# Performance work log

Hardware: AMD Instinct MI355X
Metric: run time of the kernel (lower is better)

The kernel has to match this reference:

```python
import jax, jax.numpy as jnp
import numpy as np

B, S, T, D, H, K, F = 8, 512, 512, 1024, 16, 64, 4096
EPS = 1e-6
NEG = -1e9


def _ln(x, g, b):
    mu = jnp.mean(x, axis=-1, keepdims=True)
    var = jnp.mean(jnp.square(x - mu), axis=-1, keepdims=True)
    return (x - mu) * jax.lax.rsqrt(var + EPS) * g + b


def _mha(q_in, kv_in, wq, bq, wk, bk, wv, bv, wo, bo, mask=None):
    # q_in: [B,S,D], kv_in: [B,T,D]
    q = jnp.einsum('bsd,dhk->bshk', q_in, wq) + bq
    k = jnp.einsum('btd,dhk->bthk', kv_in, wk) + bk
    v = jnp.einsum('btd,dhk->bthk', kv_in, wv) + bv
    scores = jnp.einsum('bshk,bthk->bhst', q, k) / jnp.sqrt(jnp.float32(K))
    if mask is not None:
        scores = jnp.where(mask, scores, NEG)
    attn = jax.nn.softmax(scores, axis=-1)  # [B,H,S,T]
    ctx = jnp.einsum('bhst,bthk->bshk', attn, v)
    out = jnp.einsum('bshk,hkd->bsd', ctx, wo) + bo
    return out, attn


def setup_inputs() -> dict:
    key = jax.random.key(0)
    ks = jax.random.split(key, 24)
    r = lambda i, shape: 0.02 * jax.random.normal(ks[i], shape, dtype=jnp.float32)
    inp = {
        'x': jax.random.normal(ks[0], (B, S, D), dtype=jnp.float32),
        'enc_output': jax.random.normal(ks[1], (B, T, D), dtype=jnp.float32),
        'look_ahead_mask': jnp.tril(jnp.ones((S, S), dtype=bool))[None, None],
        # mha1 (self-attention)
        'wq1': r(2, (D, H, K)), 'bq1': jnp.zeros((H, K), jnp.float32),
        'wk1': r(3, (D, H, K)), 'bk1': jnp.zeros((H, K), jnp.float32),
        'wv1': r(4, (D, H, K)), 'bv1': jnp.zeros((H, K), jnp.float32),
        'wo1': r(5, (H, K, D)), 'bo1': jnp.zeros((D,), jnp.float32),
        # mha2 (cross-attention)
        'wq2': r(6, (D, H, K)), 'bq2': jnp.zeros((H, K), jnp.float32),
        'wk2': r(7, (D, H, K)), 'bk2': jnp.zeros((H, K), jnp.float32),
        'wv2': r(8, (D, H, K)), 'bv2': jnp.zeros((H, K), jnp.float32),
        'wo2': r(9, (H, K, D)), 'bo2': jnp.zeros((D,), jnp.float32),
        # layernorms
        'g1': jnp.ones((D,), jnp.float32), 'be1': jnp.zeros((D,), jnp.float32),
        'g2': jnp.ones((D,), jnp.float32), 'be2': jnp.zeros((D,), jnp.float32),
        'g3': jnp.ones((D,), jnp.float32), 'be3': jnp.zeros((D,), jnp.float32),
        # ffn
        'w_fc1': r(10, (D, F)), 'b_fc1': jnp.zeros((F,), jnp.float32),
        'w_fc2': r(11, (F, D)), 'b_fc2': jnp.zeros((D,), jnp.float32),
    }
    return inp


def reference(x, enc_output, look_ahead_mask,
              wq1, bq1, wk1, bk1, wv1, bv1, wo1, bo1,
              wq2, bq2, wk2, bk2, wv2, bv2, wo2, bo2,
              g1, be1, g2, be2, g3, be3,
              w_fc1, b_fc1, w_fc2, b_fc2):
    attn1, attn_w1 = _mha(x, x, wq1, bq1, wk1, bk1, wv1, bv1, wo1, bo1,
                          mask=look_ahead_mask)
    out1 = _ln(attn1 + x, g1, be1)
    attn2, attn_w2 = _mha(out1, enc_output, wq2, bq2, wk2, bk2, wv2, bv2, wo2, bo2)
    out2 = _ln(attn2 + out1, g2, be2)
    h = jax.nn.relu(jnp.einsum('bsd,df->bsf', out2, w_fc1) + b_fc1)
    out_ffn = jnp.einsum('bsf,fd->bsd', h, w_fc2) + b_fc2
    dec_layer_out = _ln(out_ffn + out2, g3, be3)
    return dec_layer_out, attn_w1, attn_w2
```

## Files before the change

### kernel.cpp

```cpp
#include <hip/hip_runtime.h>

typedef __attribute__((ext_vector_type(4))) float f32x4;
typedef __attribute__((ext_vector_type(8))) __bf16 bf16x8;

__device__ __forceinline__ unsigned short f2b(float f){
  union { float f; unsigned int u; } v; v.f = f;
  unsigned int r = v.u + 0x7FFFu + ((v.u >> 16) & 1u);
  return (unsigned short)(r >> 16);
}
__device__ __forceinline__ float b2f(unsigned short u){
  union { unsigned int u; float f; } v; v.u = ((unsigned int)u) << 16;
  return v.f;
}
__device__ __forceinline__ bool in_is_bf16(const void* g1){
  return ((const unsigned short*)g1)[0] == 0x3F80u;
}

#define GLD16(gp, lp) __builtin_amdgcn_global_load_lds( \
    (const __attribute__((address_space(1))) unsigned int*)(gp), \
    (__attribute__((address_space(3))) unsigned int*)(lp), 16, 0, 0)

__device__ __forceinline__ int xcd_swz(int L, int nwg){
  return (L & 7) * (nwg >> 3) + (L >> 3);
}

__global__ __launch_bounds__(256) void k_fill(float* p, long long n, float v){
  long long i = (long long)blockIdx.x*256 + threadIdx.x;
  long long stride = (long long)gridDim.x*256;
  for(; i < n; i += stride) p[i] = v;
}

struct SmallConv { const void* src[16]; int n[16]; int off[16]; };
struct TW4 { const void* s[4]; };

template<bool SMALL>
__global__ __launch_bounds__(256) void k_prepA(SmallConv sc, float* bias,
    const void* act_in, unsigned short* act_out,
    TW4 tw, unsigned short* wdst, const void* g1f)
{
  __shared__ float tile[32][33];
  bool isb = in_is_bf16(g1f);
  int bi = blockIdx.x, tid = threadIdx.x;
  int base = SMALL ? 16 : 0;
  if(SMALL && bi < 16){
    const void* s = sc.src[bi];
    float* d = bias + sc.off[bi];
    int n = sc.n[bi];
    for(int j=tid;j<n;j+=256)
      d[j] = isb ? b2f(((const unsigned short*)s)[j]) : ((const float*)s)[j];
  } else if(bi < base + 2048){
    for(int i=(bi-base)*256+tid; i<4194304; i+=2048*256){
      float v = isb ? b2f(((const unsigned short*)act_in)[i]) : ((const float*)act_in)[i];
      act_out[i] = f2b(v);
    }
  } else {
    int r = bi - (base + 2048);
    int wi = r >> 10, rem = r & 1023;
    int c0 = (rem & 31)*32, r0 = (rem >> 5)*32;
    const void* src = tw.s[wi];
    unsigned short* dst = wdst + (size_t)wi*1048576;
    int tx = tid & 31, ty = tid >> 5;
    for(int rr=ty; rr<32; rr+=8){
      size_t o = (size_t)(r0+rr)*1024 + c0 + tx;
      tile[rr][tx] = isb ? b2f(((const unsigned short*)src)[o]) : ((const float*)src)[o];
    }
    __syncthreads();
    for(int cc=ty; cc<32; cc+=8)
      dst[(size_t)(c0+cc)*1024 + r0 + tx] = f2b(tile[tx][cc]);
  }
}

__global__ __launch_bounds__(256) void k_prep3(
    const void* fc1, unsigned short* fc1t,
    const void* fc2, unsigned short* fc2t, const void* g1f)
{
  __shared__ float tile[32][33];
  bool isb = in_is_bf16(g1f);
  int bi = blockIdx.x, tid = threadIdx.x;
  const void* src; unsigned short* dst; int R, C, bx, by;
  if(bi < 4096){ src = fc1; dst = fc1t; R = 1024; C = 4096; bx = bi & 127; by = bi >> 7; }
  else { int r = bi - 4096; src = fc2; dst = fc2t; R = 4096; C = 1024; bx = r & 31; by = r >> 5; }
  int c0 = bx*32, r0 = by*32;
  int tx = tid & 31, ty = tid >> 5;
  for(int rr=ty; rr<32; rr+=8){
    size_t o = (size_t)(r0+rr)*C + c0 + tx;
    tile[rr][tx] = isb ? b2f(((const unsigned short*)src)[o]) : ((const float*)src)[o];
  }
  __syncthreads();
  for(int cc=ty; cc<32; cc+=8)
    dst[(size_t)(c0+cc)*R + r0 + tx] = f2b(tile[tx][cc]);
}

template<int EPI>
__global__ __launch_bounds__(256) void k_gemm(
    const unsigned short* __restrict__ A, int lda,
    const unsigned short* __restrict__ Bt, int ldb,
    void* __restrict__ Cout, int ldc,
    const float* __restrict__ bias, const unsigned short* __restrict__ resid, int K)
{
  __shared__ unsigned short As[2][128*32];
  __shared__ unsigned short Bs[2][128*32];
  int tid = threadIdx.x;
  int lane = tid & 63, w = tid >> 6;
  int lr = lane & 15, lg = lane >> 4;
  int nwg = gridDim.x * gridDim.y;
  int v = xcd_swz(blockIdx.y * gridDim.x + blockIdx.x, nwg);
  int bx = v % gridDim.x, by = v / gridDim.x;
  int m0 = by * 128, n0 = bx * 128;
  int wr = w >> 1, wc = w & 1;

  f32x4 acc[4][4];
  #pragma unroll
  for(int m=0;m<4;m++)
    #pragma unroll
    for(int n=0;n<4;n++) acc[m][n] = (f32x4){0.f,0.f,0.f,0.f};

  #pragma unroll
  for(int j=0;j<2;j++){
    int idx = j*256 + tid;
    GLD16(A + (size_t)(m0 + (idx>>2))*lda + (idx&3)*8,
          As[0] + (size_t)(j*256 + (tid & 192))*8);
    GLD16(Bt + (size_t)(n0 + (idx>>2))*ldb + (idx&3)*8,
          Bs[0] + (size_t)(j*256 + (tid & 192))*8);
  }
  __syncthreads();

  int cur = 0;
  for(int k0 = 0; k0 < K; k0 += 32){
    if(k0 + 32 < K){
      #pragma unroll
      for(int j=0;j<2;j++){
        int idx = j*256 + tid;
        GLD16(A + (size_t)(m0 + (idx>>2))*lda + k0 + 32 + (idx&3)*8,
              As[cur^1] + (size_t)(j*256 + (tid & 192))*8);
        GLD16(Bt + (size_t)(n0 + (idx>>2))*ldb + k0 + 32 + (idx&3)*8,
              Bs[cur^1] + (size_t)(j*256 + (tid & 192))*8);
      }
    }
    bf16x8 a[4], b[4];
    #pragma unroll
    for(int m=0;m<4;m++) a[m] = *(const bf16x8*)&As[cur][(wr*64 + m*16 + lr)*32 + lg*8];
    #pragma unroll
    for(int n=0;n<4;n++) b[n] = *(const bf16x8*)&Bs[cur][(wc*64 + n*16 + lr)*32 + lg*8];
    #pragma unroll
    for(int m=0;m<4;m++)
      #pragma unroll
      for(int n=0;n<4;n++)
        acc[m][n] = __builtin_amdgcn_mfma_f32_16x16x32_bf16(a[m], b[n], acc[m][n], 0,0,0);
    __syncthreads();
    cur ^= 1;
  }

  #pragma unroll
  for(int m=0;m<4;m++){
    #pragma unroll
    for(int n=0;n<4;n++){
      int col = n0 + wc*64 + n*16 + lr;
      float bb = bias[col];
      #pragma unroll
      for(int r=0;r<4;r++){
        int row = m0 + wr*64 + m*16 + lg*4 + r;
        size_t o = (size_t)row*ldc + col;
        float v2 = acc[m][n][r] + bb;
        if constexpr (EPI == 0){
          ((unsigned short*)Cout)[o] = f2b(v2);
        } else if constexpr (EPI == 1){
          ((unsigned short*)Cout)[o] = f2b(v2 > 0.f ? v2 : 0.f);
        } else if constexpr (EPI == 2){
          ((unsigned short*)Cout)[o] = f2b(v2 + b2f(resid[o]));
        } else {
          ((float*)Cout)[o] = v2 + b2f(resid[o]);
        }
      }
    }
  }
}

template<int EPI>
__global__ __launch_bounds__(256) void k_gemm64(
    const unsigned short* __restrict__ A, int lda,
    const unsigned short* __restrict__ Bt, int ldb,
    void* __restrict__ Cout, int ldc,
    const float* __restrict__ bias, const unsigned short* __restrict__ resid, int K)
{
  __shared__ unsigned short As[2][128*32];
  __shared__ unsigned short Bs[2][64*32];
  int tid = threadIdx.x, lane = tid & 63, w = tid >> 6;
  int lr = lane & 15, lg = lane >> 4;
  int nwg = gridDim.x * gridDim.y;
  int v = xcd_swz(blockIdx.y * gridDim.x + blockIdx.x, nwg);
  int bx = v % gridDim.x, by = v / gridDim.x;
  int m0 = by * 128, n0 = bx * 64;

  f32x4 acc[2][4];
  #pragma unroll
  for(int m=0;m<2;m++)
    #pragma unroll
    for(int n=0;n<4;n++) acc[m][n] = (f32x4){0.f,0.f,0.f,0.f};

  #pragma unroll
  for(int j=0;j<2;j++){
    int idx = j*256 + tid;
    GLD16(A + (size_t)(m0 + (idx>>2))*lda + (idx&3)*8,
          As[0] + (size_t)(j*256 + (tid & 192))*8);
  }
  GLD16(Bt + (size_t)(n0 + (tid>>2))*ldb + (tid&3)*8,
        Bs[0] + (size_t)(tid & 192)*8);
  __syncthreads();

  int cur = 0;
  for(int k0 = 0; k0 < K; k0 += 32){
    if(k0 + 32 < K){
      #pragma unroll
      for(int j=0;j<2;j++){
        int idx = j*256 + tid;
        GLD16(A + (size_t)(m0 + (idx>>2))*lda + k0 + 32 + (idx&3)*8,
              As[cur^1] + (size_t)(j*256 + (tid & 192))*8);
      }
      GLD16(Bt + (size_t)(n0 + (tid>>2))*ldb + k0 + 32 + (tid&3)*8,
            Bs[cur^1] + (size_t)(tid & 192)*8);
    }
    bf16x8 a[2], bf[4];
    #pragma unroll
    for(int m=0;m<2;m++) a[m] = *(const bf16x8*)&As[cur][(w*32 + m*16 + lr)*32 + lg*8];
    #pragma unroll
    for(int n=0;n<4;n++) bf[n] = *(const bf16x8*)&Bs[cur][(n*16 + lr)*32 + lg*8];
    #pragma unroll
    for(int m=0;m<2;m++)
      #pragma unroll
      for(int n=0;n<4;n++)
        acc[m][n] = __builtin_amdgcn_mfma_f32_16x16x32_bf16(a[m], bf[n], acc[m][n], 0,0,0);
    __syncthreads();
    cur ^= 1;
  }

  #pragma unroll
  for(int m=0;m<2;m++){
    #pragma unroll
    for(int n=0;n<4;n++){
      int col = n0 + n*16 + lr;
      float bb = bias[col];
      #pragma unroll
      for(int r=0;r<4;r++){
        int row = m0 + w*32 + m*16 + lg*4 + r;
        size_t o = (size_t)row*ldc + col;
        float v2 = acc[m][n][r] + bb;
        if constexpr (EPI == 0){
          ((unsigned short*)Cout)[o] = f2b(v2);
        } else if constexpr (EPI == 1){
          ((unsigned short*)Cout)[o] = f2b(v2 > 0.f ? v2 : 0.f);
        } else if constexpr (EPI == 2){
          ((unsigned short*)Cout)[o] = f2b(v2 + b2f(resid[o]));
        } else {
          ((float*)Cout)[o] = v2 + b2f(resid[o]);
        }
      }
    }
  }
}

template<int TSLOT>
__global__ __launch_bounds__(256) void k_gemmsplit(
    const unsigned short* __restrict__ A, int lda,
    const unsigned short* __restrict__ Bt, int ldb,
    unsigned short* __restrict__ C0, unsigned short* __restrict__ C1,
    unsigned short* __restrict__ C2,
    const float* __restrict__ bias, int K)
{
  __shared__ unsigned short As[2][128*32];
  __shared__ unsigned short Bs[2][128*32];
  int tid = threadIdx.x;
  int lane = tid & 63, w = tid >> 6;
  int lr = lane & 15, lg = lane >> 4;
  int nwg = gridDim.x * gridDim.y;
  int v = xcd_swz(blockIdx.y * gridDim.x + blockIdx.x, nwg);
  int bx = v % gridDim.x, by = v / gridDim.x;
  int m0 = by * 128, n0 = bx * 128;
  int wr = w >> 1, wc = w & 1;
  int slot = n0 >> 10;
  unsigned short* Cs = slot == 0 ? C0 : (slot == 1 ? C1 : C2);
  int nl0 = n0 & 1023;

  f32x4 acc[4][4];
  #pragma unroll
  for(int m=0;m<4;m++)
    #pragma unroll
    for(int n=0;n<4;n++) acc[m][n] = (f32x4){0.f,0.f,0.f,0.f};

  #pragma unroll
  for(int j=0;j<2;j++){
    int idx = j*256 + tid;
    GLD16(A + (size_t)(m0 + (idx>>2))*lda + (idx&3)*8,
          As[0] + (size_t)(j*256 + (tid & 192))*8);
    GLD16(Bt + (size_t)(n0 + (idx>>2))*ldb + (idx&3)*8,
          Bs[0] + (size_t)(j*256 + (tid & 192))*8);
  }
  __syncthreads();

  int cur = 0;
  for(int k0 = 0; k0 < K; k0 += 32){
    if(k0 + 32 < K){
      #pragma unroll
      for(int j=0;j<2;j++){
        int idx = j*256 + tid;
        GLD16(A + (size_t)(m0 + (idx>>2))*lda + k0 + 32 + (idx&3)*8,
              As[cur^1] + (size_t)(j*256 + (tid & 192))*8);
        GLD16(Bt + (size_t)(n0 + (idx>>2))*ldb + k0 + 32 + (idx&3)*8,
              Bs[cur^1] + (size_t)(j*256 + (tid & 192))*8);
      }
    }
    bf16x8 a[4], b[4];
    #pragma unroll
    for(int m=0;m<4;m++) a[m] = *(const bf16x8*)&As[cur][(wr*64 + m*16 + lr)*32 + lg*8];
    #pragma unroll
    for(int n=0;n<4;n++) b[n] = *(const bf16x8*)&Bs[cur][(wc*64 + n*16 + lr)*32 + lg*8];
    #pragma unroll
    for(int m=0;m<4;m++)
      #pragma unroll
      for(int n=0;n<4;n++)
        acc[m][n] = __builtin_amdgcn_mfma_f32_16x16x32_bf16(a[m], b[n], acc[m][n], 0,0,0);
    __syncthreads();
    cur ^= 1;
  }

  if(slot != TSLOT){
    #pragma unroll
    for(int m=0;m<4;m++){
      #pragma unroll
      for(int n=0;n<4;n++){
        int coll = nl0 + wc*64 + n*16 + lr;
        float bb = bias[n0 + wc*64 + n*16 + lr];
        #pragma unroll
        for(int r=0;r<4;r++){
          int row = m0 + wr*64 + m*16 + lg*4 + r;
          Cs[(size_t)row*1024 + coll] = f2b(acc[m][n][r] + bb);
        }
      }
    }
  } else {
    #pragma unroll
    for(int m=0;m<4;m++){
      #pragma unroll
      for(int n=0;n<4;n++){
        int vcol = nl0 + wc*64 + n*16 + lr;
        float bb = bias[n0 + wc*64 + n*16 + lr];
        int rowb = m0 + wr*64 + m*16 + lg*4;
        int z = (rowb >> 9)*16 + (vcol >> 6);
        unsigned short tmp[4];
        #pragma unroll
        for(int r=0;r<4;r++) tmp[r] = f2b(acc[m][n][r] + bb);
        *(ushort4*)&Cs[((size_t)(z*64 + (vcol & 63)))*512 + (rowb & 511)] = *(ushort4*)tmp;
      }
    }
  }
}

template<bool CAUSAL>
__global__ __launch_bounds__(256) void k_attnf(
    const unsigned short* Q,
    const unsigned short* __restrict__ Km,
    const unsigned short* __restrict__ Vt,
    float* __restrict__ P,
    unsigned short* C)
{
  int tid = threadIdx.x, lane = tid & 63, w = tid >> 6;
  int lr = lane & 15, lg = lane >> 4;
  int L = (blockIdx.z * 16 + blockIdx.y) * 16 + blockIdx.x;
  int v = xcd_swz(L, 2048);
  int s0 = (v & 15) * 32;
  int h = (v >> 4) & 15;
  int b = v >> 8;
  int z = b*16 + h;
  const unsigned short* Qb = Q + ((size_t)(b*512 + s0))*1024 + h*64;
  const unsigned short* Kb = Km + ((size_t)(b*512))*1024 + h*64;
  float* Pb = P + ((size_t)(z*512 + s0))*512;

  __shared__ unsigned short P_lds[32*520];
  __shared__ float redm[32][4];
  __shared__ float reds[32][4];

  bf16x8 aq[2][2];
  #pragma unroll
  for(int m=0;m<2;m++)
    #pragma unroll
    for(int kk=0;kk<2;kk++)
      aq[m][kk] = *(const bf16x8*)(Qb + (size_t)(m*16 + lr)*1024 + kk*32 + lg*8);

  f32x4 sc[2][8];
  #pragma unroll
  for(int m=0;m<2;m++)
    #pragma unroll
    for(int cb=0;cb<8;cb++) sc[m][cb] = (f32x4){0.f,0.f,0.f,0.f};

  #pragma unroll
  for(int cb=0; cb<8; cb++){
    int col = w*128 + cb*16 + lr;
    #pragma unroll
    for(int kk=0; kk<2; kk++){
      bf16x8 bq = *(const bf16x8*)(Kb + (size_t)col*1024 + kk*32 + lg*8);
      #pragma unroll
      for(int m=0;m<2;m++)
        sc[m][cb] = __builtin_amdgcn_mfma_f32_16x16x32_bf16(aq[m][kk], bq, sc[m][cb], 0,0,0);
    }
  }

  #pragma unroll
  for(int m=0;m<2;m++)
    #pragma unroll
    for(int cb=0;cb<8;cb++)
      #pragma unroll
      for(int r=0;r<4;r++){
        int row_l = m*16 + lg*4 + r;
        int col = w*128 + cb*16 + lr;
        float sv = sc[m][cb][r] * 0.125f;
        if(CAUSAL && col > s0 + row_l) sv = -1e9f;
        sc[m][cb][r] = sv;
      }

  float gmax[2][4];
  #pragma unroll
  for(int m=0;m<2;m++)
    #pragma unroll
    for(int r=0;r<4;r++){
      float pm = -1e30f;
      #pragma unroll
      for(int cb=0;cb<8;cb++) pm = fmaxf(pm, sc[m][cb][r]);
      #pragma unroll
      for(int off=1; off<16; off<<=1) pm = fmaxf(pm, __shfl_xor(pm, off));
      if(lr == 0) redm[m*16 + lg*4 + r][w] = pm;
    }
  __syncthreads();
  #pragma unroll
  for(int m=0;m<2;m++)
    #pragma unroll
    for(int r=0;r<4;r++){
      int row_l = m*16 + lg*4 + r;
      gmax[m][r] = fmaxf(fmaxf(redm[row_l][0], redm[row_l][1]),
                         fmaxf(redm[row_l][2], redm[row_l][3]));
    }
  #pragma unroll
  for(int m=0;m<2;m++)
    #pragma unroll
    for(int r=0;r<4;r++){
      float ps = 0.f;
      #pragma unroll
      for(int cb=0;cb<8;cb++){
        float e = __expf(sc[m][cb][r] - gmax[m][r]);
        sc[m][cb][r] = e;
        ps += e;
      }
      #pragma unroll
      for(int off=1; off<16; off<<=1) ps += __shfl_xor(ps, off);
      if(lr == 0) reds[m*16 + lg*4 + r][w] = ps;
    }
  __syncthreads();
  #pragma unroll
  for(int m=0;m<2;m++)
    #pragma unroll
    for(int r=0;r<4;r++){
      int row_l = m*16 + lg*4 + r;
      float inv = 1.f / (reds[row_l][0] + reds[row_l][1] + reds[row_l][2] + reds[row_l][3]);
      #pragma unroll
      for(int cb=0;cb<8;cb++){
        int col = w*128 + cb*16 + lr;
        float p = sc[m][cb][r] * inv;
        Pb[(size_t)row_l*512 + col] = p;
        P_lds[row_l*520 + col] = f2b(p);
      }
    }
  __syncthreads();

  const unsigned short* Vb = Vt + ((size_t)z*64 + w*16 + lr)*512;
  f32x4 pacc[2];
  pacc[0] = (f32x4){0.f,0.f,0.f,0.f};
  pacc[1] = (f32x4){0.f,0.f,0.f,0.f};
  for(int kk = 0; kk < 16; kk++){
    bf16x8 bfrag = *(const bf16x8*)(Vb + kk*32 + lg*8);
    #pragma unroll
    for(int m=0;m<2;m++){
      bf16x8 afrag = *(const bf16x8*)&P_lds[(m*16 + lr)*520 + kk*32 + lg*8];
      pacc[m] = __builtin_amdgcn_mfma_f32_16x16x32_bf16(afrag, bfrag, pacc[m], 0,0,0);
    }
  }
  #pragma unroll
  for(int m=0;m<2;m++)
    #pragma unroll
    for(int r=0;r<4;r++)
      C[((size_t)(b*512 + s0 + m*16 + lg*4 + r))*1024 + h*64 + w*16 + lr] = f2b(pacc[m][r]);
}

template<int F32IN, int F32OUT>
__global__ __launch_bounds__(256) void k_ln(const void* __restrict__ in,
    const float* __restrict__ g, const float* __restrict__ be,
    void* __restrict__ out)
{
  int row = blockIdx.x, tid = threadIdx.x;
  float v[4];
  if constexpr (F32IN){
    f32x4 u = *(const f32x4*)((const float*)in + (size_t)row*1024 + tid*4);
    v[0]=u[0]; v[1]=u[1]; v[2]=u[2]; v[3]=u[3];
  } else {
    uint2 u = *(const uint2*)((const unsigned short*)in + (size_t)row*1024 + tid*4);
    v[0] = b2f(u.x & 0xFFFF); v[1] = b2f(u.x >> 16);
    v[2] = b2f(u.y & 0xFFFF); v[3] = b2f(u.y >> 16);
  }
  float s = v[0]+v[1]+v[2]+v[3];
  float s2 = v[0]*v[0]+v[1]*v[1]+v[2]*v[2]+v[3]*v[3];
  #pragma unroll
  for(int off=1; off<64; off<<=1){ s += __shfl_xor(s, off); s2 += __shfl_xor(s2, off); }
  __shared__ float red[2][4];
  int w = tid >> 6;
  if((tid & 63) == 0){ red[0][w] = s; red[1][w] = s2; }
  __syncthreads();
  s  = red[0][0]+red[0][1]+red[0][2]+red[0][3];
  s2 = red[1][0]+red[1][1]+red[1][2]+red[1][3];
  float mu = s * (1.f/1024.f);
  float var = s2 * (1.f/1024.f) - mu*mu;
  float rstd = rsqrtf(var + 1e-6f);
  int c = tid*4;
  float y0 = (v[0]-mu)*rstd*g[c+0] + be[c+0];
  float y1 = (v[1]-mu)*rstd*g[c+1] + be[c+1];
  float y2 = (v[2]-mu)*rstd*g[c+2] + be[c+2];
  float y3 = (v[3]-mu)*rstd*g[c+3] + be[c+3];
  if constexpr (F32OUT){
    f32x4 o = {y0, y1, y2, y3};
    *(f32x4*)((float*)out + (size_t)row*1024 + c) = o;
  } else {
    unsigned int o0 = (unsigned int)f2b(y0) | ((unsigned int)f2b(y1) << 16);
    unsigned int o1 = (unsigned int)f2b(y2) | ((unsigned int)f2b(y3) << 16);
    *(uint2*)((unsigned short*)out + (size_t)row*1024 + c) = make_uint2(o0, o1);
  }
}

extern "C" void kernel_launch(void* const* d_in, const int* in_sizes, int n_in,
                              void* d_out, int out_size, void* d_ws, size_t ws_size,
                              hipStream_t stream)
{
  float* out0 = (float*)d_out;

  static const int exp_sizes[29] = {
    4194304, 4194304, 262144,
    1048576, 1024, 1048576, 1024, 1048576, 1024, 1048576, 1024,
    1048576, 1024, 1048576, 1024, 1048576, 1024, 1048576, 1024,
    1024, 1024, 1024, 1024, 1024, 1024,
    4194304, 4096, 4194304, 1024 };
  bool ok = (n_in == 29);
  if(ok) for(int i=0;i<29;i++) if(in_sizes[i] != exp_sizes[i]) { ok = false; break; }
  if(!ok){
    k_fill<<<2048,256,0,stream>>>(out0, (long long)out_size, 100.0f);
    return;
  }
  size_t nslots = ws_size > 131072 ? (ws_size - 131072) / 8388608 : 0;
  if(nslots < 5){
    k_fill<<<2048,256,0,stream>>>(out0, (long long)out_size, 200.0f);
    return;
  }
  bool bigws = nslots >= 9;

  const void* g1f = d_in[19];
  char* ws = (char*)d_ws;
  float* bias = (float*)(ws);
  unsigned short* SL[9];
  for(int i=0;i<9;i++) SL[i] = (unsigned short*)(ws + 131072 + (size_t)i*8388608);

  float* P1 = out0 + 4194304;
  float* P2 = P1 + 33554432;

  SmallConv scv;
  const int si[16] = {4,6,8,10,12,14,16,18,19,20,21,22,23,24,26,28};
  const int sn[16] = {1024,1024,1024,1024,1024,1024,1024,1024,
                      1024,1024,1024,1024,1024,1024,4096,1024};
  const int so[16] = {0,1024,2048,3072,4096,5120,6144,7168,
                      8192,9216,10240,11264,12288,13312,14336,18432};
  for(int i=0;i<16;i++){ scv.src[i]=d_in[si[i]]; scv.n[i]=sn[i]; scv.off[i]=so[i]; }

  {
    TW4 tw{}; tw.s[0]=d_in[3]; tw.s[1]=d_in[5]; tw.s[2]=d_in[7]; tw.s[3]=d_in[9];
    k_prepA<true><<<6160,256,0,stream>>>(scv, bias, d_in[0], SL[0], tw, SL[1], g1f);
  }
  k_gemmsplit<2><<<dim3(24,32),256,0,stream>>>(SL[0],1024, SL[1],1024,
                                               SL[2], SL[3], SL[4], bias+0, 1024);
  k_attnf<true><<<dim3(16,16,8),256,0,stream>>>(SL[2], SL[3], SL[4], P1, SL[2]);
  k_gemm64<2><<<dim3(16,32),256,0,stream>>>(SL[2],1024, SL[1]+3145728,1024,
                                            SL[3],1024, bias+3072, SL[0], 1024);
  k_ln<0,0><<<4096,256,0,stream>>>(SL[3], bias+8192, bias+9216, SL[4]);

  {
    TW4 tw{}; tw.s[0]=d_in[11]; tw.s[1]=d_in[13]; tw.s[2]=d_in[15]; tw.s[3]=d_in[17];
    k_prepA<false><<<6144,256,0,stream>>>(scv, bias, d_in[1], SL[0], tw, SL[1], g1f);
  }
  k_gemmsplit<1><<<dim3(16,32),256,0,stream>>>(SL[0],1024, SL[1]+1048576,1024,
                                               SL[2], SL[3], nullptr, bias+5120, 1024);
  k_gemm64<0><<<dim3(16,32),256,0,stream>>>(SL[4],1024, SL[1],1024,
                                            SL[0],1024, bias+4096, nullptr, 1024);
  k_attnf<false><<<dim3(16,16,8),256,0,stream>>>(SL[0], SL[2], SL[3], P2, SL[0]);
  k_gemm64<2><<<dim3(16,32),256,0,stream>>>(SL[0],1024, SL[1]+3145728,1024,
                                            SL[2],1024, bias+7168, SL[4], 1024);
  k_ln<0,0><<<4096,256,0,stream>>>(SL[2], bias+10240, bias+11264, SL[3]);

  k_prep3<<<8192,256,0,stream>>>(d_in[25], SL[4], d_in[27], SL[0], g1f);
  if(bigws){
    unsigned short* H = SL[5];
    k_gemm<1><<<dim3(32,32),256,0,stream>>>(SL[3],1024, SL[4],1024, H,4096, bias+14336, nullptr, 1024);
    k_gemm64<3><<<dim3(16,32),256,0,stream>>>(H,4096, SL[0],4096, out0,1024, bias+18432, SL[3], 4096);
    k_ln<1,1><<<4096,256,0,stream>>>(out0, bias+12288, bias+13312, out0);
  } else {
    unsigned short* H = SL[1];
    for(int c=0;c<2;c++){
      unsigned short* arow = SL[3] + (size_t)c*2097152;
      float* orow = out0 + (size_t)c*2097152;
      k_gemm<1><<<dim3(32,16),256,0,stream>>>(arow,1024, SL[4],1024, H,4096, bias+14336, nullptr, 1024);
      k_gemm64<3><<<dim3(16,16),256,0,stream>>>(H,4096, SL[0],4096, orow,1024, bias+18432, arow, 4096);
      k_ln<1,1><<<2048,256,0,stream>>>(orow, bias+12288, bias+13312, orow);
    }
  }
}
```

Baseline: 471.2 us.

## Use 256x256 pipelined FFN GEMM, merge cross-attn Q/KV projections, add setprio

Replaces the 128x128 FC1 GEMM with a 512-thread 256x256-tile kernel. It uses a 64-wide K step, XOR-swizzled LDS, staged loads interleaved with the MFMA phases, and s_setprio around the MFMA blocks. The cross-attention Q projection is folded into the K/V split GEMM by letting slot 0 read a different A operand, which saves one launch; the Q result is written into the output buffer as scratch. Attention kernels also get setprio raised around their MFMA loops. The larger tiles cut global traffic per FLOP, but they produce fewer workgroups (256 for the FC1 GEMM) and use more LDS and registers.

New measurement: 473.5 us. Within noise of the previous version (+0.5%).

```diff
diff --git a/kernel.cpp b/kernel.cpp
--- a/kernel.cpp
+++ b/kernel.cpp
@@ -92,74 +92,113 @@
 }
 
 template<int EPI>
-__global__ __launch_bounds__(256) void k_gemm(
+__global__ __launch_bounds__(512) void k_gemm256(
     const unsigned short* __restrict__ A, int lda,
     const unsigned short* __restrict__ Bt, int ldb,
     void* __restrict__ Cout, int ldc,
     const float* __restrict__ bias, const unsigned short* __restrict__ resid, int K)
 {
-  __shared__ unsigned short As[2][128*32];
-  __shared__ unsigned short Bs[2][128*32];
+  __shared__ __align__(16) unsigned short LA[2][256*64];
+  __shared__ __align__(16) unsigned short LB[2][256*64];
   int tid = threadIdx.x;
-  int lane = tid & 63, w = tid >> 6;
+  int lane = tid & 63;
   int lr = lane & 15, lg = lane >> 4;
+  int w = tid >> 6, wr = w >> 2, wc = w & 3;
   int nwg = gridDim.x * gridDim.y;
   int v = xcd_swz(blockIdx.y * gridDim.x + blockIdx.x, nwg);
   int bx = v % gridDim.x, by = v / gridDim.x;
-  int m0 = by * 128, n0 = bx * 128;
-  int wr = w >> 1, wc = w & 1;
-
-  f32x4 acc[4][4];
-  #pragma unroll
-  for(int m=0;m<4;m++)
+  int m0 = by * 256, n0 = bx * 256;
+  int NT = K >> 6;
+
+  f32x4 acc[8][4];
+  #pragma unroll
+  for(int m=0;m<8;m++)
     #pragma unroll
     for(int n=0;n<4;n++) acc[m][n] = (f32x4){0.f,0.f,0.f,0.f};
 
-  #pragma unroll
-  for(int j=0;j<2;j++){
-    int idx = j*256 + tid;
-    GLD16(A + (size_t)(m0 + (idx>>2))*lda + (idx&3)*8,
-          As[0] + (size_t)(j*256 + (tid & 192))*8);
-    GLD16(Bt + (size_t)(n0 + (idx>>2))*ldb + (idx&3)*8,
-          Bs[0] + (size_t)(j*256 + (tid & 192))*8);
-  }
-  __syncthreads();
-
-  int cur = 0;
-  for(int k0 = 0; k0 < K; k0 += 32){
-    if(k0 + 32 < K){
-      #pragma unroll
-      for(int j=0;j<2;j++){
-        int idx = j*256 + tid;
-        GLD16(A + (size_t)(m0 + (idx>>2))*lda + k0 + 32 + (idx&3)*8,
-              As[cur^1] + (size_t)(j*256 + (tid & 192))*8);
-        GLD16(Bt + (size_t)(n0 + (idx>>2))*ldb + k0 + 32 + (idx&3)*8,
-              Bs[cur^1] + (size_t)(j*256 + (tid & 192))*8);
-      }
-    }
-    bf16x8 a[4], b[4];
-    #pragma unroll
-    for(int m=0;m<4;m++) a[m] = *(const bf16x8*)&As[cur][(wr*64 + m*16 + lr)*32 + lg*8];
-    #pragma unroll
-    for(int n=0;n<4;n++) b[n] = *(const bf16x8*)&Bs[cur][(wc*64 + n*16 + lr)*32 + lg*8];
-    #pragma unroll
-    for(int m=0;m<4;m++)
-      #pragma unroll
-      for(int n=0;n<4;n++)
-        acc[m][n] = __builtin_amdgcn_mfma_f32_16x16x32_bf16(a[m], b[n], acc[m][n], 0,0,0);
-    __syncthreads();
-    cur ^= 1;
-  }
-
-  #pragma unroll
-  for(int m=0;m<4;m++){
+  #define STEP256(kt, sg) { \
+    int sb_ = (kt) & 1; \
+    _Pragma("unroll") \
+    for(int jj=0;jj<2;jj++){ \
+      int c_ = (((sg)&1)*2 + jj)*512 + tid; \
+      int s_ = c_ ^ ((c_ >> 3) & 7); \
+      if(((sg) & 2) == 0) \
+        GLD16(A + (size_t)(m0 + (s_>>3))*lda + (kt)*64 + (s_&7)*8, \
+              LA[sb_] + (size_t)c_*8); \
+      else \
+        GLD16(Bt + (size_t)(n0 + (s_>>3))*ldb + (kt)*64 + (s_&7)*8, \
+              LB[sb_] + (size_t)c_*8); \
+    } }
+
+  #pragma unroll
+  for(int sg=0;sg<4;sg++) STEP256(0, sg);
+  if(NT > 1){
+    #pragma unroll
+    for(int sg=0;sg<4;sg++) STEP256(1, sg);
+    asm volatile("s_waitcnt vmcnt(8)" ::: "memory");
+  } else {
+    asm volatile("s_waitcnt vmcnt(0)" ::: "memory");
+  }
+  __builtin_amdgcn_s_barrier();
+
+  for(int kt = 0; kt < NT; ++kt){
+    int cur = kt & 1;
+    #pragma unroll
+    for(int q=0;q<4;q++){
+      bf16x8 afr[2][2], bfr[4][2];
+      #pragma unroll
+      for(int i=0;i<2;i++){
+        int row = wr*128 + (2*q+i)*16 + lr;
+        #pragma unroll
+        for(int ks=0;ks<2;ks++){
+          int ch = (row*8 + ks*4 + lg) ^ (row & 7);
+          afr[i][ks] = *(const bf16x8*)(LA[cur] + (size_t)ch*8);
+        }
+      }
+      #pragma unroll
+      for(int n=0;n<4;n++){
+        int row = wc*64 + n*16 + lr;
+        #pragma unroll
+        for(int ks=0;ks<2;ks++){
+          int ch = (row*8 + ks*4 + lg) ^ (row & 7);
+          bfr[n][ks] = *(const bf16x8*)(LB[cur] + (size_t)ch*8);
+        }
+      }
+      int P = kt*4 + q;
+      if(P >= 3){
+        int k2 = (P+5) >> 2, sg = (P+5) & 3;
+        if(k2 < NT) STEP256(k2, sg);
+      }
+      __builtin_amdgcn_s_barrier();
+      __builtin_amdgcn_s_setprio(1);
+      #pragma unroll
+      for(int i=0;i<2;i++)
+        #pragma unroll
+        for(int n=0;n<4;n++)
+          #pragma unroll
+          for(int ks=0;ks<2;ks++)
+            acc[2*q+i][n] = __builtin_amdgcn_mfma_f32_16x16x32_bf16(
+                afr[i][ks], bfr[n][ks], acc[2*q+i][n], 0,0,0);
+      __builtin_amdgcn_s_setprio(0);
+      __builtin_amdgcn_s_barrier();
+    }
+    if(kt + 1 < NT){
+      if(kt + 2 < NT) asm volatile("s_waitcnt vmcnt(2)" ::: "memory");
+      else            asm volatile("s_waitcnt vmcnt(0)" ::: "memory");
+      __builtin_amdgcn_s_barrier();
+    }
+  }
+  #undef STEP256
+
+  #pragma unroll
+  for(int m=0;m<8;m++){
     #pragma unroll
     for(int n=0;n<4;n++){
       int col = n0 + wc*64 + n*16 + lr;
       float bb = bias[col];
       #pragma unroll
       for(int r=0;r<4;r++){
-        int row = m0 + wr*64 + m*16 + lg*4 + r;
+        int row = m0 + wr*128 + m*16 + lg*4 + r;
         size_t o = (size_t)row*ldc + col;
         float v2 = acc[m][n][r] + bb;
         if constexpr (EPI == 0){
@@ -261,7 +300,8 @@
 
 template<int TSLOT>
 __global__ __launch_bounds__(256) void k_gemmsplit(
-    const unsigned short* __restrict__ A, int lda,
+    const unsigned short* __restrict__ A,
+    const unsigned short* __restrict__ A2, int lda,
     const unsigned short* __restrict__ Bt, int ldb,
     unsigned short* __restrict__ C0, unsigned short* __restrict__ C1,
     unsigned short* __restrict__ C2,
@@ -279,6 +319,7 @@
   int wr = w >> 1, wc = w & 1;
   int slot = n0 >> 10;
   unsigned short* Cs = slot == 0 ? C0 : (slot == 1 ? C1 : C2);
+  const unsigned short* Au = (slot == 0) ? A2 : A;
   int nl0 = n0 & 1023;
 
   f32x4 acc[4][4];
@@ -290,7 +331,7 @@
   #pragma unroll
   for(int j=0;j<2;j++){
     int idx = j*256 + tid;
-    GLD16(A + (size_t)(m0 + (idx>>2))*lda + (idx&3)*8,
+    GLD16(Au + (size_t)(m0 + (idx>>2))*lda + (idx&3)*8,
           As[0] + (size_t)(j*256 + (tid & 192))*8);
     GLD16(Bt + (size_t)(n0 + (idx>>2))*ldb + (idx&3)*8,
           Bs[0] + (size_t)(j*256 + (tid & 192))*8);
@@ -303,7 +344,7 @@
       #pragma unroll
       for(int j=0;j<2;j++){
         int idx = j*256 + tid;
-        GLD16(A + (size_t)(m0 + (idx>>2))*lda + k0 + 32 + (idx&3)*8,
+        GLD16(Au + (size_t)(m0 + (idx>>2))*lda + k0 + 32 + (idx&3)*8,
               As[cur^1] + (size_t)(j*256 + (tid & 192))*8);
         GLD16(Bt + (size_t)(n0 + (idx>>2))*ldb + k0 + 32 + (idx&3)*8,
               Bs[cur^1] + (size_t)(j*256 + (tid & 192))*8);
@@ -392,6 +433,7 @@
     #pragma unroll
     for(int cb=0;cb<8;cb++) sc[m][cb] = (f32x4){0.f,0.f,0.f,0.f};
 
+  __builtin_amdgcn_s_setprio(1);
   #pragma unroll
   for(int cb=0; cb<8; cb++){
     int col = w*128 + cb*16 + lr;
@@ -403,6 +445,7 @@
         sc[m][cb] = __builtin_amdgcn_mfma_f32_16x16x32_bf16(aq[m][kk], bq, sc[m][cb], 0,0,0);
     }
   }
+  __builtin_amdgcn_s_setprio(0);
 
   #pragma unroll
   for(int m=0;m<2;m++)
@@ -474,6 +517,7 @@
   f32x4 pacc[2];
   pacc[0] = (f32x4){0.f,0.f,0.f,0.f};
   pacc[1] = (f32x4){0.f,0.f,0.f,0.f};
+  __builtin_amdgcn_s_setprio(1);
   for(int kk = 0; kk < 16; kk++){
     bf16x8 bfrag = *(const bf16x8*)(Vb + kk*32 + lg*8);
     #pragma unroll
@@ -482,6 +526,7 @@
       pacc[m] = __builtin_amdgcn_mfma_f32_16x16x32_bf16(afrag, bfrag, pacc[m], 0,0,0);
     }
   }
+  __builtin_amdgcn_s_setprio(0);
   #pragma unroll
   for(int m=0;m<2;m++)
     #pragma unroll
@@ -565,6 +610,7 @@
 
   float* P1 = out0 + 4194304;
   float* P2 = P1 + 33554432;
+  unsigned short* Q2buf = (unsigned short*)out0;
 
   SmallConv scv;
   const int si[16] = {4,6,8,10,12,14,16,18,19,20,21,22,23,24,26,28};
@@ -578,7 +624,7 @@
     TW4 tw{}; tw.s[0]=d_in[3]; tw.s[1]=d_in[5]; tw.s[2]=d_in[7]; tw.s[3]=d_in[9];
     k_prepA<true><<<6160,256,0,stream>>>(scv, bias, d_in[0], SL[0], tw, SL[1], g1f);
   }
-  k_gemmsplit<2><<<dim3(24,32),256,0,stream>>>(SL[0],1024, SL[1],1024,
+  k_gemmsplit<2><<<dim3(24,32),256,0,stream>>>(SL[0], SL[0],1024, SL[1],1024,
                                                SL[2], SL[3], SL[4], bias+0, 1024);
   k_attnf<true><<<dim3(16,16,8),256,0,stream>>>(SL[2], SL[3], SL[4], P1, SL[2]);
   k_gemm64<2><<<dim3(16,32),256,0,stream>>>(SL[2],1024, SL[1]+3145728,1024,
@@ -589,11 +635,9 @@
     TW4 tw{}; tw.s[0]=d_in[11]; tw.s[1]=d_in[13]; tw.s[2]=d_in[15]; tw.s[3]=d_in[17];
     k_prepA<false><<<6144,256,0,stream>>>(scv, bias, d_in[1], SL[0], tw, SL[1], g1f);
   }
-  k_gemmsplit<1><<<dim3(16,32),256,0,stream>>>(SL[0],1024, SL[1]+1048576,1024,
-                                               SL[2], SL[3], nullptr, bias+5120, 1024);
-  k_gemm64<0><<<dim3(16,32),256,0,stream>>>(SL[4],1024, SL[1],1024,
-                                            SL[0],1024, bias+4096, nullptr, 1024);
-  k_attnf<false><<<dim3(16,16,8),256,0,stream>>>(SL[0], SL[2], SL[3], P2, SL[0]);
+  k_gemmsplit<2><<<dim3(24,32),256,0,stream>>>(SL[0], SL[4],1024, SL[1],1024,
+                                               Q2buf, SL[2], SL[3], bias+4096, 1024);
+  k_attnf<false><<<dim3(16,16,8),256,0,stream>>>(Q2buf, SL[2], SL[3], P2, SL[0]);
   k_gemm64<2><<<dim3(16,32),256,0,stream>>>(SL[0],1024, SL[1]+3145728,1024,
                                             SL[2],1024, bias+7168, SL[4], 1024);
   k_ln<0,0><<<4096,256,0,stream>>>(SL[2], bias+10240, bias+11264, SL[3]);
@@ -601,7 +645,8 @@
   k_prep3<<<8192,256,0,stream>>>(d_in[25], SL[4], d_in[27], SL[0], g1f);
   if(bigws){
     unsigned short* H = SL[5];
-    k_gemm<1><<<dim3(32,32),256,0,stream>>>(SL[3],1024, SL[4],1024, H,4096, bias+14336, nullptr, 1024);
+    k_gemm256<1><<<dim3(16,16),512,0,stream>>>(SL[3],1024, SL[4],1024, H,4096,
+                                               bias+14336, nullptr, 1024);
     k_gemm64<3><<<dim3(16,32),256,0,stream>>>(H,4096, SL[0],4096, out0,1024, bias+18432, SL[3], 4096);
     k_ln<1,1><<<4096,256,0,stream>>>(out0, bias+12288, bias+13312, out0);
   } else {
@@ -609,7 +654,8 @@
     for(int c=0;c<2;c++){
       unsigned short* arow = SL[3] + (size_t)c*2097152;
       float* orow = out0 + (size_t)c*2097152;
-      k_gemm<1><<<dim3(32,16),256,0,stream>>>(arow,1024, SL[4],1024, H,4096, bias+14336, nullptr, 1024);
+      k_gemm256<1><<<dim3(16,8),512,0,stream>>>(arow,1024, SL[4],1024, H,4096,
+                                                bias+14336, nullptr, 1024);
       k_gemm64<3><<<dim3(16,16),256,0,stream>>>(H,4096, SL[0],4096, orow,1024, bias+18432, arow, 4096);
       k_ln<1,1><<<2048,256,0,stream>>>(orow, bias+12288, bias+13312, orow);
     }
```
